# Kernel optimization log

Hardware: AMD Instinct MI355X
Metric: run time of the kernel (lower is better)

The kernel has to match this reference:

```python
import jax, jax.numpy as jnp
import numpy as np

NB_COMP = 8
LAT_DIM = 512
NB_NEUR = 1024
OUT_DIM = 512
N_SAMPLES = 16384


def setup_inputs() -> dict:
    key = jax.random.key(0)
    ks = jax.random.split(key, 8)
    s1 = 1.0 / np.sqrt(LAT_DIM)
    s2 = 1.0 / np.sqrt(NB_NEUR)
    return {
        "epsilon": jax.random.normal(ks[0], (N_SAMPLES, LAT_DIM), dtype=jnp.float32),
        "comp_idx": jax.random.randint(ks[1], (N_SAMPLES,), 0, NB_COMP, dtype=jnp.int32),
        "mu": jnp.zeros((NB_COMP, LAT_DIM), dtype=jnp.float32),
        "rho": jnp.zeros((NB_COMP,), dtype=jnp.float32),  # sigma = softplus(rho)
        "W1": jax.random.normal(ks[2], (NB_COMP, LAT_DIM, NB_NEUR), dtype=jnp.float32) * s1,
        "b1": jax.random.normal(ks[3], (NB_COMP, NB_NEUR), dtype=jnp.float32) * s1,
        "W2": jax.random.normal(ks[4], (NB_COMP, NB_NEUR, OUT_DIM), dtype=jnp.float32) * s2,
        "b2": jax.random.normal(ks[5], (NB_COMP, OUT_DIM), dtype=jnp.float32) * s2,
    }


def reference(epsilon, comp_idx, mu, rho, W1, b1, W2, b2):
    # GNNens.forward: per-sample categorical component dispatch through a
    # 1-hidden-layer sigmoid MLP. Vectorized as compute-all-components + select.
    sigma = jax.nn.softplus(rho)                          # [C]
    # lat_c[c,n,d] = epsilon[n,d] * sigma[c] + mu[c,d]
    lat = epsilon[None, :, :] * sigma[:, None, None] + mu[:, None, :]  # [C,N,D]
    h = jax.nn.sigmoid(jnp.einsum('cnd,cdh->cnh', lat, W1) + b1[:, None, :])  # [C,N,H]
    y = jnp.einsum('cnh,cho->cno', h, W2) + b2[:, None, :]                    # [C,N,O]
    # select each sample's routed component
    idx = comp_idx[None, :, None].astype(jnp.int32)       # [1,N,1]
    out = jnp.take_along_axis(y, idx, axis=0)[0]          # [N,O]
    return out
```

## Files before the change

kernel.cpp:

```cpp
#include <hip/hip_runtime.h>
#include <stdint.h>

#define NCOMP 8
#define LATD  512
#define HID   1024
#define OUTD  512
#define NS    16384

typedef unsigned short u16;
typedef __bf16 bf16x8 __attribute__((ext_vector_type(8)));
typedef float  f32x4  __attribute__((ext_vector_type(4)));

#define MAPS       (NS/128 + NCOMP)
#define SLOT_CHUNK ((MAPS + 7)/8)

#define ORDER_OFF  2048
#define APACK_OFF  (ORDER_OFF + NS*4)
#define W1T_OFF    (APACK_OFF + (size_t)NS*LATD*2)
#define W2T_OFF    (W1T_OFF + (size_t)NCOMP*LATD*HID*2)
#define H_OFF      (W2T_OFF + (size_t)NCOMP*HID*OUTD*2)
#define WS_NEEDED  (H_OFF + (size_t)NS*HID*2)

#define PACK_B0   8
#define PACK_NB   2048
#define W1T_B0    (PACK_B0 + PACK_NB)
#define PREP_NB   (W1T_B0 + 1024)
#define G1_JOBS   (8*SLOT_CHUNK*(HID/128))

__device__ __forceinline__ u16 f2b(float f) {
  unsigned int u = __builtin_bit_cast(unsigned int, f);
  u = (u + 0x7FFFu + ((u >> 16) & 1u)) >> 16;
  return (u16)u;
}

__device__ __forceinline__ void load_lds16(const void* g, void* l) {
  __builtin_amdgcn_global_load_lds((const __attribute__((address_space(1))) void*)g,
                                   (__attribute__((address_space(3))) void*)l, 16, 0, 0);
}

__device__ __forceinline__
void wtrans64(const float* __restrict__ src, u16* __restrict__ dst,
              int CC, int R, int c0, int r0, float* tile ) {
  const int t = threadIdx.x;
  const int tx = t & 63, ty = t >> 6;
  for (int rr = ty; rr < 64; rr += 4)
    tile[rr*65 + tx] = src[(size_t)(r0+rr)*CC + c0 + tx];
  __syncthreads();
  const int ch = t & 15;
  #pragma unroll
  for (int q = 0; q < 4; ++q) {
    const int cc = (t >> 4) + (q << 4);
    float f0 = tile[((ch<<2)+0)*65 + cc];
    float f1 = tile[((ch<<2)+1)*65 + cc];
    float f2 = tile[((ch<<2)+2)*65 + cc];
    float f3 = tile[((ch<<2)+3)*65 + cc];
    uint2 pk;
    pk.x = (unsigned)f2b(f0) | ((unsigned)f2b(f1) << 16);
    pk.y = (unsigned)f2b(f2) | ((unsigned)f2b(f3) << 16);
    *reinterpret_cast<uint2*>(&dst[(size_t)(c0+cc)*R + r0 + (ch<<2)]) = pk;
  }
}

__global__ __launch_bounds__(256)
void k_prep(const int* __restrict__ idx, const float* __restrict__ rho,
            const float* __restrict__ eps, const float* __restrict__ mu,
            const float* __restrict__ W1,
            int* __restrict__ offsets, int* __restrict__ ntiles,
            int* __restrict__ map, int* __restrict__ order,
            u16* __restrict__ Apack, u16* __restrict__ W1T) {
  __shared__ float tile[64*65];
  __shared__ int hist_s[NCOMP];
  __shared__ int wtot[4];
  const int b = blockIdx.x;
  const int t = threadIdx.x;

  if (b < NCOMP) {
    const int c = b;
    const int wave = t >> 6, lane = t & 63;
    unsigned long long lo = 0, hi = 0;
    for (int i = 0; i < 64; ++i) {
      int v = idx[t + (i << 8)];
      unsigned long long one = 1ull << ((v & 3) << 4);
      if (v < 4) lo += one; else hi += one;
    }
    if (t < NCOMP) hist_s[t] = 0;
    __syncthreads();

    unsigned long long rlo = lo, rhi = hi;
    #pragma unroll
    for (int d = 1; d < 64; d <<= 1) { rlo += __shfl_xor(rlo, d); rhi += __shfl_xor(rhi, d); }
    if (lane == 0) {
      #pragma unroll
      for (int cc = 0; cc < 4; ++cc) atomicAdd(&hist_s[cc],   (int)((rlo >> (cc<<4)) & 0xffff));
      #pragma unroll
      for (int cc = 0; cc < 4; ++cc) atomicAdd(&hist_s[cc+4], (int)((rhi >> (cc<<4)) & 0xffff));
    }

    int v = (int)(((c < 4 ? lo : hi) >> ((c & 3) << 4)) & 0xffff);
    int s = v;
    #pragma unroll
    for (int d = 1; d < 64; d <<= 1) { int u = __shfl_up(s, d); if (lane >= d) s += u; }
    if (lane == 63) wtot[wave] = s;
    __syncthreads();

    int wbase = 0;
    for (int w = 0; w < wave; ++w) wbase += wtot[w];
    int off_c = 0;
    #pragma unroll
    for (int cc = 0; cc < NCOMP; ++cc) if (cc < c) off_c += hist_s[cc];

    int pos = off_c + wbase + (s - v);
    for (int i = 0; i < 64; ++i) {
      int smp = t + (i << 8);
      if (idx[smp] == c) order[pos++] = smp;
    }

    if (t == 0) {
      if (c == 0) {
        int a = 0;
        for (int cc = 0; cc < NCOMP; ++cc) { offsets[cc] = a; a += hist_s[cc]; }
        offsets[NCOMP] = a;
        int tot = 0;
        for (int cc = 0; cc < NCOMP; ++cc) tot += (hist_s[cc] + 127) >> 7;
        ntiles[0] = tot;
      }
      int mb = 0;
      for (int cc = 0; cc < c; ++cc) mb += (hist_s[cc] + 127) >> 7;
      int nt = (hist_s[c] + 127) >> 7;
      for (int m = 0; m < nt; ++m) map[mb + m] = (c << 16) | m;
    }
  } else if (b < W1T_B0) {
    const int base = (b - PACK_B0) << 3;
    #pragma unroll
    for (int it = 0; it < 2; ++it) {
      int i = base + (it << 2) + (t >> 6);
      int d = (t & 63) << 3;
      int c = idx[i];
      float r = rho[c];
      float sg = (r > 20.f) ? r : log1pf(expf(r));
      const float4* ep = reinterpret_cast<const float4*>(eps + (size_t)i*LATD + d);
      const float4* mp = reinterpret_cast<const float4*>(mu  + (size_t)c*LATD + d);
      float4 e0 = ep[0], e1 = ep[1], m0 = mp[0], m1 = mp[1];
      unsigned o0 = f2b(e0.x*sg+m0.x), o1 = f2b(e0.y*sg+m0.y), o2 = f2b(e0.z*sg+m0.z), o3 = f2b(e0.w*sg+m0.w);
      unsigned o4 = f2b(e1.x*sg+m1.x), o5 = f2b(e1.y*sg+m1.y), o6 = f2b(e1.z*sg+m1.z), o7 = f2b(e1.w*sg+m1.w);
      uint4 pk;
      pk.x = o0 | (o1<<16); pk.y = o2 | (o3<<16); pk.z = o4 | (o5<<16); pk.w = o6 | (o7<<16);
      *reinterpret_cast<uint4*>(Apack + (size_t)i*LATD + d) = pk;
    }
  } else {
    int bb = b - W1T_B0;
    int comp = bb >> 7, loc = bb & 127;
    wtrans64(W1 + (size_t)comp*LATD*HID, W1T + (size_t)comp*LATD*HID,
             HID, LATD, (loc & 15) << 6, (loc >> 4) << 6, tile);
  }
}

template<int K, int NB, int STAGE>
__device__ __forceinline__
void gemm_tile(const int id, const u16* __restrict__ A, const u16* __restrict__ BT,
               const int* __restrict__ offsets, const int* __restrict__ ntiles,
               const int* __restrict__ map, const int* __restrict__ order,
               const float* __restrict__ bias,
               u16* __restrict__ Hout, float* __restrict__ Yout,
               u16* As, u16* Bs, int* ord) {
  constexpr int NCB = NB/128;
  const int xcd   = id & 7;
  const int sub   = id >> 3;
  const int ncolb = sub % NCB;
  const int slot  = xcd*SLOT_CHUNK + sub / NCB;
  if (slot >= ntiles[0]) return;
  const int packed = map[slot];
  const int c      = packed >> 16;
  const int bstart = offsets[c];
  const int bend   = offsets[c+1];
  const int tile0  = bstart + (packed & 0xffff)*128;
  const int ncol0  = ncolb*128;

  const int tid  = threadIdx.x;
  const int wave = tid >> 6;
  const int lane = tid & 63;
  const int srow = (wave<<5) + (lane>>3);
  const int scol = ((lane & 7) ^ ((lane >> 3) & 7)) << 3;

  if (STAGE == 2 && tid < 128) {
    int gr = tile0 + tid;
    ord[tid] = order[gr < bend ? gr : bstart];
  }

  size_t a_off[4], b_off[4];
  const size_t bbase = (size_t)c * NB * K;
  #pragma unroll
  for (int i = 0; i < 4; ++i) {
    int ar = tile0 + srow + (i<<3);
    if (ar >= bend) ar = bend - 1;
    int arow = (STAGE == 1) ? order[ar] : ar;
    a_off[i] = (size_t)arow * K + scol;
    b_off[i] = bbase + (size_t)(ncol0 + srow + (i<<3)) * K + scol;
  }

  const int wr   = (wave >> 1) << 6;
  const int wc   = (wave & 1) << 6;
  const int quad = lane >> 4;
  const int l16  = lane & 15;
  const int sw   = l16 & 7;

  f32x4 acc[4][4] = {};

  for (int k0 = 0; k0 < K; k0 += 64) {
    #pragma unroll
    for (int i = 0; i < 4; ++i)
      load_lds16(A + a_off[i] + k0, &As[((wave<<5) + (i<<3))<<6]);
    #pragma unroll
    for (int i = 0; i < 4; ++i)
      load_lds16(BT + b_off[i] + k0, &Bs[((wave<<5) + (i<<3))<<6]);
    __syncthreads();
    #pragma unroll
    for (int kk = 0; kk < 64; kk += 32) {
      const int kc = (kk >> 3) + quad;
      const int sc = (kc ^ sw) << 3;
      bf16x8 af[4], bfr[4];
      #pragma unroll
      for (int mi = 0; mi < 4; ++mi)
        af[mi] = *reinterpret_cast<const bf16x8*>(&As[((wr + (mi<<4) + l16)<<6) + sc]);
      #pragma unroll
      for (int ni = 0; ni < 4; ++ni)
        bfr[ni] = *reinterpret_cast<const bf16x8*>(&Bs[((wc + (ni<<4) + l16)<<6) + sc]);
      #pragma unroll
      for (int ni = 0; ni < 4; ++ni)
        #pragma unroll
        for (int mi = 0; mi < 4; ++mi)
          acc[ni][mi] = __builtin_amdgcn_mfma_f32_16x16x32_bf16(bfr[ni], af[mi], acc[ni][mi], 0, 0, 0);
    }
    __syncthreads();
  }

  f32x4 bias4[4];
  #pragma unroll
  for (int ni = 0; ni < 4; ++ni)
    bias4[ni] = *reinterpret_cast<const f32x4*>(
        &bias[(size_t)c*NB + ncol0 + wc + (ni<<4) + (quad<<2)]);

  #pragma unroll
  for (int mi = 0; mi < 4; ++mi) {
    const int row_l = wr + (mi<<4) + l16;
    const int grow  = tile0 + row_l;
    if (grow < bend) {
      #pragma unroll
      for (int ni = 0; ni < 4; ++ni) {
        const int col = ncol0 + wc + (ni<<4) + (quad<<2);
        float v0 = acc[ni][mi][0] + bias4[ni][0];
        float v1 = acc[ni][mi][1] + bias4[ni][1];
        float v2 = acc[ni][mi][2] + bias4[ni][2];
        float v3 = acc[ni][mi][3] + bias4[ni][3];
        if (STAGE == 1) {
          v0 = __builtin_amdgcn_rcpf(1.0f + __expf(-v0));
          v1 = __builtin_amdgcn_rcpf(1.0f + __expf(-v1));
          v2 = __builtin_amdgcn_rcpf(1.0f + __expf(-v2));
          v3 = __builtin_amdgcn_rcpf(1.0f + __expf(-v3));
          uint2 pk;
          pk.x = (unsigned)f2b(v0) | ((unsigned)f2b(v1) << 16);
          pk.y = (unsigned)f2b(v2) | ((unsigned)f2b(v3) << 16);
          *reinterpret_cast<uint2*>(&Hout[(size_t)grow*NB + col]) = pk;
        } else {
          float4 o; o.x = v0; o.y = v1; o.z = v2; o.w = v3;
          *reinterpret_cast<float4*>(&Yout[(size_t)ord[row_l]*NB + col]) = o;
        }
      }
    }
  }
}

union __attribute__((aligned(16))) SmemU {
  struct { u16 As[128*64]; u16 Bs[128*64]; } g;
  float tile[64*65];
};

__global__ __launch_bounds__(256, 4)
void k_g1w2t(const u16* __restrict__ Apack, const u16* __restrict__ W1T,
             const float* __restrict__ W2,
             const int* __restrict__ offsets, const int* __restrict__ ntiles,
             const int* __restrict__ map, const int* __restrict__ order,
             const float* __restrict__ b1,
             u16* __restrict__ Hout, u16* __restrict__ W2T) {
  __shared__ SmemU sm;
  __shared__ int ord[128];
  const int id = blockIdx.x;
  if (id < G1_JOBS) {
    gemm_tile<LATD, HID, 1>(id, Apack, W1T, offsets, ntiles, map, order, b1,
                            Hout, nullptr, sm.g.As, sm.g.Bs, ord);
  } else {
    int bb = id - G1_JOBS;
    int comp = bb >> 7, loc = bb & 127;
    wtrans64(W2 + (size_t)comp*HID*OUTD, W2T + (size_t)comp*HID*OUTD,
             OUTD, HID, (loc & 7) << 6, (loc >> 3) << 6, sm.tile);
  }
}

__global__ __launch_bounds__(256, 4)
void k_gemm2(const u16* __restrict__ Hws, const u16* __restrict__ W2T,
             const int* __restrict__ offsets, const int* __restrict__ ntiles,
             const int* __restrict__ map, const int* __restrict__ order,
             const float* __restrict__ b2, float* __restrict__ Yout) {
  __shared__ __attribute__((aligned(16))) u16 As[128*64];
  __shared__ __attribute__((aligned(16))) u16 Bs[128*64];
  __shared__ int ord[128];
  gemm_tile<HID, OUTD, 2>(blockIdx.x, Hws, W2T, offsets, ntiles, map, order, b2,
                          nullptr, Yout, As, Bs, ord);
}

__global__ void k_naive(const float* __restrict__ eps, const int* __restrict__ idx,
                        const float* __restrict__ mu, const float* __restrict__ rho,
                        const float* __restrict__ W1, const float* __restrict__ b1,
                        const float* __restrict__ W2, const float* __restrict__ b2,
                        float* __restrict__ out) {
  __shared__ float lat[LATD];
  __shared__ float h[HID];
  int n = blockIdx.x, t = threadIdx.x;
  int c = idx[n];
  float r = rho[c];
  float sg = (r > 20.f) ? r : log1pf(expf(r));
  for (int d = t; d < LATD; d += 256) lat[d] = eps[(size_t)n*LATD+d]*sg + mu[(size_t)c*LATD+d];
  __syncthreads();
  for (int j = t; j < HID; j += 256) {
    float a = b1[(size_t)c*HID+j];
    const float* w = W1 + (size_t)c*LATD*HID + j;
    for (int d = 0; d < LATD; ++d) a += lat[d]*w[(size_t)d*HID];
    h[j] = 1.f/(1.f+expf(-a));
  }
  __syncthreads();
  for (int o = t; o < OUTD; o += 256) {
    float a = b2[(size_t)c*OUTD+o];
    const float* w = W2 + (size_t)c*HID*OUTD + o;
    for (int j = 0; j < HID; ++j) a += h[j]*w[(size_t)j*OUTD];
    out[(size_t)n*OUTD+o] = a;
  }
}

extern "C" void kernel_launch(void* const* d_in, const int* in_sizes, int n_in,
                              void* d_out, int out_size, void* d_ws, size_t ws_size,
                              hipStream_t stream) {
  const float* eps = (const float*)d_in[0];
  const int*   idx = (const int*)d_in[1];
  const float* mu  = (const float*)d_in[2];
  const float* rho = (const float*)d_in[3];
  const float* W1  = (const float*)d_in[4];
  const float* b1  = (const float*)d_in[5];
  const float* W2  = (const float*)d_in[6];
  const float* b2  = (const float*)d_in[7];
  float* out = (float*)d_out;

  if (ws_size < WS_NEEDED) {
    k_naive<<<NS, 256, 0, stream>>>(eps, idx, mu, rho, W1, b1, W2, b2, out);
    return;
  }

  char* ws = (char*)d_ws;
  int*   offsets = (int*)(ws + 0);
  int*   ntiles  = (int*)(ws + 96);
  int*   map     = (int*)(ws + 128);
  int*   order   = (int*)(ws + ORDER_OFF);
  u16*   Apack   = (u16*)(ws + APACK_OFF);
  u16*   W1T     = (u16*)(ws + W1T_OFF);
  u16*   W2T     = (u16*)(ws + W2T_OFF);
  u16*   Hws     = (u16*)(ws + H_OFF);

  k_prep<<<PREP_NB, 256, 0, stream>>>(
      idx, rho, eps, mu, W1, offsets, ntiles, map, order, Apack, W1T);
  k_g1w2t<<<G1_JOBS + 1024, 256, 0, stream>>>(
      Apack, W1T, W2, offsets, ntiles, map, order, b1, Hws, W2T);
  k_gemm2<<<8*SLOT_CHUNK*(OUTD/128), 256, 0, stream>>>(
      Hws, W2T, offsets, ntiles, map, order, b2, out);
}
```

Baseline: 196.2 us.

## Move W2 transpose into prep kernel and cap gemm1 grid at 1024 blocks

Measured after the change: 190.2 us. 1.03x faster.

```diff
diff --git a/kernel.cpp b/kernel.cpp
--- a/kernel.cpp
+++ b/kernel.cpp
@@ -24,8 +24,11 @@
 #define PACK_B0   8
 #define PACK_NB   2048
 #define W1T_B0    (PACK_B0 + PACK_NB)
-#define PREP_NB   (W1T_B0 + 1024)
+#define W2T_B0    (W1T_B0 + 1024)
+#define PREP_NB   (W2T_B0 + 1024)
+
 #define G1_JOBS   (8*SLOT_CHUNK*(HID/128))
+#define G2_JOBS   (8*SLOT_CHUNK*(OUTD/128))
 
 __device__ __forceinline__ u16 f2b(float f) {
   unsigned int u = __builtin_bit_cast(unsigned int, f);
@@ -64,10 +67,10 @@
 __global__ __launch_bounds__(256)
 void k_prep(const int* __restrict__ idx, const float* __restrict__ rho,
             const float* __restrict__ eps, const float* __restrict__ mu,
-            const float* __restrict__ W1,
+            const float* __restrict__ W1, const float* __restrict__ W2,
             int* __restrict__ offsets, int* __restrict__ ntiles,
             int* __restrict__ map, int* __restrict__ order,
-            u16* __restrict__ Apack, u16* __restrict__ W1T) {
+            u16* __restrict__ Apack, u16* __restrict__ W1T, u16* __restrict__ W2T) {
   __shared__ float tile[64*65];
   __shared__ int hist_s[NCOMP];
   __shared__ int wtot[4];
@@ -147,11 +150,16 @@
       pk.x = o0 | (o1<<16); pk.y = o2 | (o3<<16); pk.z = o4 | (o5<<16); pk.w = o6 | (o7<<16);
       *reinterpret_cast<uint4*>(Apack + (size_t)i*LATD + d) = pk;
     }
-  } else {
+  } else if (b < W2T_B0) {
     int bb = b - W1T_B0;
     int comp = bb >> 7, loc = bb & 127;
     wtrans64(W1 + (size_t)comp*LATD*HID, W1T + (size_t)comp*LATD*HID,
              HID, LATD, (loc & 15) << 6, (loc >> 4) << 6, tile);
+  } else {
+    int bb = b - W2T_B0;
+    int comp = bb >> 7, loc = bb & 127;
+    wtrans64(W2 + (size_t)comp*HID*OUTD, W2T + (size_t)comp*HID*OUTD,
+             OUTD, HID, (loc & 7) << 6, (loc >> 3) << 6, tile);
   }
 }
 
@@ -270,29 +278,22 @@
   }
 }
 
-union __attribute__((aligned(16))) SmemU {
-  struct { u16 As[128*64]; u16 Bs[128*64]; } g;
-  float tile[64*65];
-};
-
 __global__ __launch_bounds__(256, 4)
-void k_g1w2t(const u16* __restrict__ Apack, const u16* __restrict__ W1T,
-             const float* __restrict__ W2,
+void k_gemm1(const u16* __restrict__ Apack, const u16* __restrict__ W1T,
              const int* __restrict__ offsets, const int* __restrict__ ntiles,
              const int* __restrict__ map, const int* __restrict__ order,
-             const float* __restrict__ b1,
-             u16* __restrict__ Hout, u16* __restrict__ W2T) {
-  __shared__ SmemU sm;
+             const float* __restrict__ b1, u16* __restrict__ Hout) {
+  __shared__ __attribute__((aligned(16))) u16 As[128*64];
+  __shared__ __attribute__((aligned(16))) u16 Bs[128*64];
   __shared__ int ord[128];
-  const int id = blockIdx.x;
-  if (id < G1_JOBS) {
-    gemm_tile<LATD, HID, 1>(id, Apack, W1T, offsets, ntiles, map, order, b1,
-                            Hout, nullptr, sm.g.As, sm.g.Bs, ord);
-  } else {
-    int bb = id - G1_JOBS;
-    int comp = bb >> 7, loc = bb & 127;
-    wtrans64(W2 + (size_t)comp*HID*OUTD, W2T + (size_t)comp*HID*OUTD,
-             OUTD, HID, (loc & 7) << 6, (loc >> 3) << 6, sm.tile);
+  #pragma unroll
+  for (int j = 0; j < 2; ++j) {
+    const int id = blockIdx.x + (j << 10);
+    if (id < G1_JOBS) {
+      if (j) __syncthreads();
+      gemm_tile<LATD, HID, 1>(id, Apack, W1T, offsets, ntiles, map, order, b1,
+                              Hout, nullptr, As, Bs, ord);
+    }
   }
 }
 
@@ -365,9 +366,9 @@
   u16*   Hws     = (u16*)(ws + H_OFF);
 
   k_prep<<<PREP_NB, 256, 0, stream>>>(
-      idx, rho, eps, mu, W1, offsets, ntiles, map, order, Apack, W1T);
-  k_g1w2t<<<G1_JOBS + 1024, 256, 0, stream>>>(
-      Apack, W1T, W2, offsets, ntiles, map, order, b1, Hws, W2T);
-  k_gemm2<<<8*SLOT_CHUNK*(OUTD/128), 256, 0, stream>>>(
+      idx, rho, eps, mu, W1, W2, offsets, ntiles, map, order, Apack, W1T, W2T);
+  k_gemm1<<<1024, 256, 0, stream>>>(
+      Apack, W1T, offsets, ntiles, map, order, b1, Hws);
+  k_gemm2<<<G2_JOBS, 256, 0, stream>>>(
       Hws, W2T, offsets, ntiles, map, order, b2, out);
 }
```
